# Kernel optimization log

Hardware: AMD Instinct MI355X
Metric: run time of the kernel (lower is better)

The kernel has to match this reference:

```python
import jax, jax.numpy as jnp
import numpy as np

B, N, C, H, PD, CLN = 8, 1024, 512, 8, 256, 64
HD = C // H
HID = 4 * C
LN_EPS = 1e-5
ATT_EPS = 1e-6


def layernorm(x, g, b):
    mu = x.mean(-1, keepdims=True)
    var = ((x - mu) ** 2).mean(-1, keepdims=True)
    return (x - mu) * jax.lax.rsqrt(var + LN_EPS) * g + b


def setup_inputs() -> dict:
    key = jax.random.key(0)
    ks = jax.random.split(key, 16)
    p = lambda k, shp, s=0.02: (jax.random.normal(k, shp, dtype=jnp.float32) * s)
    return {
        "x_token": jax.random.normal(ks[0], (B, N, C), dtype=jnp.float32),
        "x_path": jax.random.normal(ks[1], (B, N, PD), dtype=jnp.float32),
        "wq": p(ks[2], (C, C)),
        "wk": p(ks[3], (C, C)),
        "wv": p(ks[4], (C, C)),
        "w_proj": p(ks[5], (C, C)),
        "b_proj": jnp.zeros((C,), jnp.float32),
        "g1": jnp.ones((C,), jnp.float32),
        "b1": jnp.zeros((C,), jnp.float32),
        "g2": jnp.ones((C,), jnp.float32),
        "b2": jnp.zeros((C,), jnp.float32),
        "w1": p(ks[6], (HID, C)),
        "bb1": jnp.zeros((HID,), jnp.float32),
        "w2": p(ks[7], (C, HID)),
        "bb2": jnp.zeros((C,), jnp.float32),
        "idx_cluster": jax.random.randint(ks[8], (B, N), 0, CLN, dtype=jnp.int64 if jax.config.jax_enable_x64 else jnp.int32),
        "cluster_num": CLN,
    }


def reference(x_token, x_path, wq, wk, wv, w_proj, b_proj, g1, b1, g2, b2,
              w1, bb1, w2, bb2, idx_cluster, cluster_num):
    Bn, Nn, Cn = x_token.shape
    scale = (Cn // H) ** -0.5

    # norm1 + attention
    t = layernorm(x_token, g1, b1)
    q = (t @ wq.T).reshape(Bn, Nn, H, HD).transpose(0, 2, 1, 3)  # bhnd
    k = (t @ wk.T).reshape(Bn, Nn, H, HD).transpose(0, 2, 1, 3)
    v = (t @ wv.T).reshape(Bn, Nn, H, HD).transpose(0, 2, 1, 3)

    # scatter-to-(B,cluster,N,C) then sum over clusters == same-cluster mask on QK^T
    scores = jnp.einsum("bhid,bhjd->bhij", q, k) * scale  # (B,H,N,N)
    same = (idx_cluster[:, None, :, None] == idx_cluster[:, None, None, :])  # (B,1,N,N)
    scores = jnp.where(same, scores, jnp.float32(-1e9))

    # custom eps-stabilized exp-softmax (as in the torch code, no max-subtraction)
    e = jnp.exp(scores.astype(jnp.float32))
    attn = (e + ATT_EPS / Nn) / (e.sum(-1, keepdims=True) + ATT_EPS)

    out = jnp.einsum("bhij,bhjd->bhid", attn, v)
    out = out.transpose(0, 2, 1, 3).reshape(Bn, Nn, Cn)
    out = out @ w_proj.T + b_proj

    x = x_token + out  # drop_path is identity in eval

    # MLP block
    h = layernorm(x, g2, b2)
    m = jax.nn.gelu(h @ w1.T + bb1, approximate=False) @ w2.T + bb2
    return x + m
```

## Files before the change

### kernel.cpp

```cpp
#include <hip/hip_runtime.h>

typedef unsigned short u16;
typedef __attribute__((ext_vector_type(4))) float f32x4;
typedef __attribute__((ext_vector_type(8))) short s16x8;
typedef __attribute__((ext_vector_type(4))) unsigned short u16x4;
typedef __attribute__((ext_vector_type(8))) unsigned short u16x8;

__device__ __forceinline__ u16 f2bf(float f) {
    unsigned int u = __builtin_bit_cast(unsigned int, f);
    u += 0x7fffu + ((u >> 16) & 1u);
    return (u16)(u >> 16);
}
__device__ __forceinline__ float bf2f(u16 h) {
    unsigned int u = ((unsigned int)h) << 16;
    return __builtin_bit_cast(float, u);
}
__device__ __forceinline__ void gload16(const u16* g, u16* l) {
    __builtin_amdgcn_global_load_lds(
        (const __attribute__((address_space(1))) void*)g,
        (__attribute__((address_space(3))) void*)l, 16, 0, 0);
}

__global__ __launch_bounds__(256) void cvt_all(const float* __restrict__ wq,
                                               const float* __restrict__ wk,
                                               const float* __restrict__ wv,
                                               const float* __restrict__ wp,
                                               const float* __restrict__ w1,
                                               const float* __restrict__ w2,
                                               u16* __restrict__ dqkv,
                                               u16* __restrict__ dp,
                                               u16* __restrict__ dw1,
                                               u16* __restrict__ dw2,
                                               float* __restrict__ vsum) {
    int b = blockIdx.x;
    if (b >= 3072) {
        float4 z = {0.f, 0.f, 0.f, 0.f};
        ((float4*)vsum)[(b - 3072) * 256 + threadIdx.x] = z;
        return;
    }
    const float* src; u16* dst; int off;
    if      (b < 256)  { src = wq; dst = dqkv;          off = b; }
    else if (b < 512)  { src = wk; dst = dqkv + 262144; off = b - 256; }
    else if (b < 768)  { src = wv; dst = dqkv + 524288; off = b - 512; }
    else if (b < 1024) { src = wp; dst = dp;            off = b - 768; }
    else if (b < 2048) { src = w1; dst = dw1;           off = b - 1024; }
    else               { src = w2; dst = dw2;           off = b - 2048; }
    int i = off * 256 + threadIdx.x;
    float4 v = ((const float4*)src)[i];
    u16x4 o;
    o.x = f2bf(v.x); o.y = f2bf(v.y); o.z = f2bf(v.z); o.w = f2bf(v.w);
    ((u16x4*)dst)[i] = o;
}

template <bool IN_BF16>
__global__ __launch_bounds__(128) void ln_kernel(const void* __restrict__ inp,
                                                 const float* __restrict__ g,
                                                 const float* __restrict__ bta,
                                                 u16* __restrict__ out) {
    int row = blockIdx.x;
    int t = threadIdx.x;
    float4 v;
    if (IN_BF16) {
        u16x4 hv = ((const u16x4*)inp)[row * 128 + t];
        v.x = bf2f(hv.x); v.y = bf2f(hv.y); v.z = bf2f(hv.z); v.w = bf2f(hv.w);
    } else {
        v = ((const float4*)inp)[row * 128 + t];
    }
    float s  = v.x + v.y + v.z + v.w;
    float s2 = v.x * v.x + v.y * v.y + v.z * v.z + v.w * v.w;
#pragma unroll
    for (int m = 1; m < 64; m <<= 1) { s += __shfl_xor(s, m); s2 += __shfl_xor(s2, m); }
    __shared__ float sh[4];
    if ((t & 63) == 0) { sh[(t >> 6) * 2] = s; sh[(t >> 6) * 2 + 1] = s2; }
    __syncthreads();
    s = sh[0] + sh[2]; s2 = sh[1] + sh[3];
    float mu  = s * (1.0f / 512.0f);
    float var = s2 * (1.0f / 512.0f) - mu * mu;
    float rstd = rsqrtf(var + 1e-5f);
    float4 gv = ((const float4*)g)[t];
    float4 bv = ((const float4*)bta)[t];
    u16x4 o;
    o.x = f2bf((v.x - mu) * rstd * gv.x + bv.x);
    o.y = f2bf((v.y - mu) * rstd * gv.y + bv.y);
    o.z = f2bf((v.z - mu) * rstd * gv.z + bv.z);
    o.w = f2bf((v.w - mu) * rstd * gv.w + bv.w);
    ((u16x4*)(out + (size_t)row * 512))[t] = o;
}

__global__ __launch_bounds__(1024) void cluster_sort(const int* __restrict__ idx,
                                                     int* __restrict__ perm,
                                                     int* __restrict__ cstart,
                                                     int* __restrict__ ccnt) {
    const int b = blockIdx.x, t = threadIdx.x;
    const int w = t >> 6, lane = t & 63;
    __shared__ int whist[16][64];
    __shared__ int cnt[64];
    __shared__ int off[64];
    ((int*)whist)[t] = 0;
    __syncthreads();
    const int myc = idx[b * 1024 + t];
    atomicAdd(&whist[w][myc], 1);
    int rank_w = 0;
    for (int c = 0; c < 64; ++c) {
        unsigned long long m = __ballot(myc == c);
        if (myc == c) rank_w = __popcll(m & ((1ull << lane) - 1ull));
    }
    __syncthreads();
    if (t < 64) {
        int s = 0;
        for (int ww = 0; ww < 16; ++ww) s += whist[ww][t];
        cnt[t] = s;
        ccnt[b * 64 + t] = s;
    }
    __syncthreads();
    if (t == 0) {
        int s = 0;
        for (int c = 0; c < 64; ++c) { off[c] = s; s += cnt[c]; }
    }
    __syncthreads();
    int cross = 0;
    for (int ww = 0; ww < w; ++ww) cross += whist[ww][myc];
    perm[b * 1024 + off[myc] + cross + rank_w] = t;
    if (t < 64) cstart[b * 64 + t] = off[t];
}

__global__ __launch_bounds__(64) void cattn_kernel(const u16* __restrict__ qkv,
                                                   const int* __restrict__ perm,
                                                   const int* __restrict__ cstart,
                                                   const int* __restrict__ ccnt,
                                                   const float* __restrict__ vsum,
                                                   u16* __restrict__ O) {
    const int bid = blockIdx.x;
    const int h = bid & 7, c = (bid >> 3) & 63, b = bid >> 9;
    const int m = ccnt[b * 64 + c];
    if (m == 0) return;
    const int start = b * 1024 + cstart[b * 64 + c];
    const int lane = threadIdx.x;
    const int fr = lane & 15, fkb = lane >> 4;
    __shared__ __align__(16) u16 Qs[16 * 72];
    __shared__ __align__(16) u16 Ks[32 * 72];
    __shared__ __align__(16) u16 Vt[64 * 36];
    __shared__ __align__(16) u16 Pl[16 * 40];

    const u16* qkv_b = qkv + (size_t)b * 1024 * 1536;
    const float epsN = 1e-6f / 1024.0f;

    for (int q0 = 0; q0 < m; q0 += 16) {
        __syncthreads();
        {
            int row = lane >> 3, seg = lane & 7;
#pragma unroll
            for (int p = 0; p < 2; ++p) {
                int r = row + p * 8;
                int gr = perm[start + min(q0 + r, m - 1)];
                *(int4*)(&Qs[r * 72 + seg * 8]) =
                    *(const int4*)(qkv_b + (size_t)gr * 1536 + h * 64 + seg * 8);
            }
        }
        __syncthreads();
        const s16x8 qf0 = *(const s16x8*)(&Qs[fr * 72 + fkb * 8]);
        const s16x8 qf1 = *(const s16x8*)(&Qs[fr * 72 + 32 + fkb * 8]);

        f32x4 oacc[4] = {};
        float rs[4] = {0.f, 0.f, 0.f, 0.f};

        for (int k0 = 0; k0 < m; k0 += 32) {
            __syncthreads();
            {
                int row = lane >> 3, seg = lane & 7;
#pragma unroll
                for (int p = 0; p < 4; ++p) {
                    int r = row + p * 8;
                    int gr = perm[start + min(k0 + r, m - 1)];
                    const u16* src = qkv_b + (size_t)gr * 1536 + h * 64 + seg * 8;
                    *(int4*)(&Ks[r * 72 + seg * 8]) = *(const int4*)(src + 512);
                    u16x8 vv = *(const u16x8*)(src + 1024);
#pragma unroll
                    for (int i = 0; i < 8; ++i) Vt[(seg * 8 + i) * 36 + r] = vv[i];
                }
            }
            __syncthreads();
#pragma unroll
            for (int ct = 0; ct < 2; ++ct) {
                f32x4 sacc = {};
                s16x8 kf0 = *(const s16x8*)(&Ks[(ct * 16 + fr) * 72 + fkb * 8]);
                s16x8 kf1 = *(const s16x8*)(&Ks[(ct * 16 + fr) * 72 + 32 + fkb * 8]);
                sacc = __builtin_amdgcn_mfma_f32_16x16x32_bf16(qf0, kf0, sacc, 0, 0, 0);
                sacc = __builtin_amdgcn_mfma_f32_16x16x32_bf16(qf1, kf1, sacc, 0, 0, 0);
                bool valid = (k0 + ct * 16 + fr) < m;
#pragma unroll
                for (int r = 0; r < 4; ++r) {
                    float e = valid ? __expf(sacc[r] * 0.125f) : 0.0f;
                    rs[r] += e;
                    Pl[(fkb * 4 + r) * 40 + ct * 16 + fr] = f2bf(e);
                }
            }
            __syncthreads();
            s16x8 pf = *(const s16x8*)(&Pl[fr * 40 + fkb * 8]);
#pragma unroll
            for (int dt = 0; dt < 4; ++dt) {
                s16x8 vf = *(const s16x8*)(&Vt[(dt * 16 + fr) * 36 + fkb * 8]);
                oacc[dt] = __builtin_amdgcn_mfma_f32_16x16x32_bf16(pf, vf, oacc[dt], 0, 0, 0);
            }
        }
#pragma unroll
        for (int r = 0; r < 4; ++r)
#pragma unroll
            for (int mm = 1; mm < 16; mm <<= 1) rs[r] += __shfl_xor(rs[r], mm);

#pragma unroll
        for (int r = 0; r < 4; ++r) {
            int ql = q0 + fkb * 4 + r;
            if (ql < m) {
                int orow = perm[start + ql];
#pragma unroll
                for (int dt = 0; dt < 4; ++dt) {
                    int dcol = dt * 16 + fr;
                    float vs = vsum[(b * 8 + h) * 64 + dcol];
                    float val = (oacc[dt][r] + epsN * vs) / (rs[r] + 1e-6f);
                    O[((size_t)(b * 1024 + orow)) * 512 + h * 64 + dcol] = f2bf(val);
                }
            }
        }
    }
}

template <int BM, int BN, bool OUT_BF16, bool BIAS, int RESID, bool GELU, bool VSUM>
__global__ __launch_bounds__(256) void gemm_sb(const u16* __restrict__ A,
                                               const u16* __restrict__ W,
                                               const float* __restrict__ bias,
                                               const void* __restrict__ resid,
                                               void* __restrict__ outp,
                                               float* __restrict__ vsum,
                                               int M, int N, int K) {
    constexpr int MI = BM / 32;
    constexpr int NI = BN / 32;
    __shared__ __align__(16) u16 As[BM * 64];
    __shared__ __align__(16) u16 Bs[BN * 64];
    const int bm = blockIdx.x, bn = blockIdx.y;
    const int t = threadIdx.x;
    const int lane = t & 63, w = t >> 6;
    const int wm = w >> 1, wn = w & 1;
    const int fr = lane & 15, fkb = lane >> 4;
    const int l8 = lane >> 3;
    const int c8s = (((lane & 7) ^ (l8 & 7)) * 8);
    f32x4 acc[MI][NI] = {};
    const u16* Ab = A + (size_t)bm * BM * K;
    const u16* Wb = W + (size_t)bn * BN * K;

    for (int k0 = 0; k0 < K; k0 += 64) {
        __syncthreads();
#pragma unroll
        for (int j = 0; j < MI; ++j) {
            int r = (w * MI + j) * 8 + l8;
            gload16(Ab + (size_t)r * K + k0 + c8s, &As[(w * MI + j) * 512]);
        }
#pragma unroll
        for (int j = 0; j < NI; ++j) {
            int r = (w * NI + j) * 8 + l8;
            gload16(Wb + (size_t)r * K + k0 + c8s, &Bs[(w * NI + j) * 512]);
        }
        __syncthreads();
#pragma unroll
        for (int kk = 0; kk < 64; kk += 32) {
            const int co = (((kk >> 3) + fkb) ^ (fr & 7)) << 3;
            s16x8 af[MI], bfv[NI];
#pragma unroll
            for (int mi = 0; mi < MI; ++mi)
                af[mi] = *(const s16x8*)(&As[(wm * (BM / 2) + mi * 16 + fr) * 64 + co]);
#pragma unroll
            for (int ni = 0; ni < NI; ++ni)
                bfv[ni] = *(const s16x8*)(&Bs[(wn * (BN / 2) + ni * 16 + fr) * 64 + co]);
#pragma unroll
            for (int mi = 0; mi < MI; ++mi)
#pragma unroll
                for (int ni = 0; ni < NI; ++ni)
                    acc[mi][ni] = __builtin_amdgcn_mfma_f32_16x16x32_bf16(
                        af[mi], bfv[ni], acc[mi][ni], 0, 0, 0);
        }
    }

    const int rg = (lane >> 4) * 4;
#pragma unroll
    for (int mi = 0; mi < MI; ++mi) {
#pragma unroll
        for (int ni = 0; ni < NI; ++ni) {
            int gcol = bn * BN + wn * (BN / 2) + ni * 16 + fr;
            float bv = BIAS ? bias[gcol] : 0.0f;
#pragma unroll
            for (int r = 0; r < 4; ++r) {
                int grow = bm * BM + wm * (BM / 2) + mi * 16 + rg + r;
                float v = acc[mi][ni][r] + bv;
                if (GELU) v = 0.5f * v * (1.0f + erff(v * 0.70710678118f));
                if (RESID == 1) v += ((const float*)resid)[(size_t)grow * N + gcol];
                if (RESID == 2) v += bf2f(((const u16*)resid)[(size_t)grow * N + gcol]);
                if (OUT_BF16)
                    ((u16*)outp)[(size_t)grow * N + gcol] = f2bf(v);
                else
                    ((float*)outp)[(size_t)grow * N + gcol] = v;
            }
        }
    }

    if (VSUM && bn * BN >= 1024) {
        const int vb = (bm * BM) >> 10;
#pragma unroll
        for (int ni = 0; ni < NI; ++ni) {
            float p = 0.0f;
#pragma unroll
            for (int mi = 0; mi < MI; ++mi)
#pragma unroll
                for (int r = 0; r < 4; ++r) p += acc[mi][ni][r];
            p += __shfl_xor(p, 16);
            p += __shfl_xor(p, 32);
            if (lane < 16) {
                int gcol = bn * BN + wn * (BN / 2) + ni * 16 + lane;
                atomicAdd(&vsum[vb * 512 + gcol - 1024], p);
            }
        }
    }
}

extern "C" void kernel_launch(void* const* d_in, const int* in_sizes, int n_in,
                              void* d_out, int out_size, void* d_ws, size_t ws_size,
                              hipStream_t stream) {
    const float* x_token = (const float*)d_in[0];
    const float* wq     = (const float*)d_in[2];
    const float* wk     = (const float*)d_in[3];
    const float* wv     = (const float*)d_in[4];
    const float* w_proj = (const float*)d_in[5];
    const float* b_proj = (const float*)d_in[6];
    const float* g1     = (const float*)d_in[7];
    const float* b1     = (const float*)d_in[8];
    const float* g2     = (const float*)d_in[9];
    const float* b2     = (const float*)d_in[10];
    const float* w1     = (const float*)d_in[11];
    const float* bb1    = (const float*)d_in[12];
    const float* w2     = (const float*)d_in[13];
    const float* bb2    = (const float*)d_in[14];
    const int*   idx    = (const int*)d_in[15];
    float* out_f = (float*)d_out;

    char* ws = (char*)d_ws;
    u16*   t_buf = (u16*)(ws);
    u16*   qkv   = (u16*)(ws + 8388608);
    u16*   Obuf  = (u16*)(ws + 8388608 + 25165824);
    u16*   m1    = qkv;
    u16*   x_bf  = (u16*)(ws + 41943040);
    u16*   h_buf = t_buf;
    char*  wsw   = ws + 58720256;
    u16*   wqkv  = (u16*)(wsw);
    u16*   wprjb = (u16*)(wsw + 1572864);
    u16*   w1b   = (u16*)(wsw + 2097152);
    u16*   w2b   = (u16*)(wsw + 4194304);
    float* vsum  = (float*)(wsw + 6291456);
    int*   perm   = (int*)(ws + 41943040);
    int*   cstart = (int*)(ws + 41943040 + 32768);
    int*   ccnt   = (int*)(ws + 41943040 + 34816);
    (void)ws_size; (void)in_sizes; (void)n_in; (void)out_size;

    cvt_all<<<3076, 256, 0, stream>>>(wq, wk, wv, w_proj, w1, w2,
                                      wqkv, wprjb, w1b, w2b, vsum);
    cluster_sort<<<8, 1024, 0, stream>>>(idx, perm, cstart, ccnt);

    ln_kernel<false><<<8192, 128, 0, stream>>>(x_token, g1, b1, t_buf);
    gemm_sb<64, 128, true, false, 0, false, true><<<dim3(128, 12), 256, 0, stream>>>(
        t_buf, wqkv, nullptr, nullptr, qkv, vsum, 8192, 1536, 512);
    cattn_kernel<<<4096, 64, 0, stream>>>(qkv, perm, cstart, ccnt, vsum, Obuf);
    gemm_sb<64, 64, true, true, 1, false, false><<<dim3(128, 8), 256, 0, stream>>>(
        Obuf, wprjb, b_proj, x_token, x_bf, nullptr, 8192, 512, 512);
    ln_kernel<true><<<8192, 128, 0, stream>>>(x_bf, g2, b2, h_buf);
    gemm_sb<64, 128, true, true, 0, true, false><<<dim3(128, 16), 256, 0, stream>>>(
        h_buf, w1b, bb1, nullptr, m1, nullptr, 8192, 2048, 512);
    gemm_sb<64, 64, false, true, 2, false, false><<<dim3(128, 8), 256, 0, stream>>>(
        m1, w2b, bb2, x_bf, out_f, nullptr, 8192, 512, 2048);
}
```

Before: 132.8 us.

## Fuse LN1 into conversion kernel, load Q directly, retile proj GEMM

Folds the first layernorm into the weight-conversion launch as extra blocks, two rows per block. These blocks also emit a bf16 copy of x_token, so the projection GEMM reads a bf16 residual and uses 32-row tiles over twice as many blocks. The attention kernel loads Q fragments straight from global memory into registers, dropping the Q shared-memory stage and two barriers per query tile. This saves a launch and some memory traffic, at the cost of rounding the first residual to bf16, which adds precision error.

```diff
diff --git a/kernel.cpp b/kernel.cpp
--- a/kernel.cpp
+++ b/kernel.cpp
@@ -31,8 +31,45 @@
                                                u16* __restrict__ dp,
                                                u16* __restrict__ dw1,
                                                u16* __restrict__ dw2,
-                                               float* __restrict__ vsum) {
+                                               float* __restrict__ vsum,
+                                               const float* __restrict__ x_token,
+                                               const float* __restrict__ g1,
+                                               const float* __restrict__ b1,
+                                               u16* __restrict__ t_out,
+                                               u16* __restrict__ xtok_bf) {
+    __shared__ float sh[4][2];
     int b = blockIdx.x;
+    if (b >= 3076) {
+        int tid = threadIdx.x;
+        int row = (b - 3076) * 2 + (tid >> 7);
+        int t = tid & 127;
+        float4 v = ((const float4*)(x_token + (size_t)row * 512))[t];
+        float s  = v.x + v.y + v.z + v.w;
+        float s2 = v.x * v.x + v.y * v.y + v.z * v.z + v.w * v.w;
+#pragma unroll
+        for (int m = 1; m < 64; m <<= 1) { s += __shfl_xor(s, m); s2 += __shfl_xor(s2, m); }
+        int w = tid >> 6;
+        if ((tid & 63) == 0) { sh[w][0] = s; sh[w][1] = s2; }
+        __syncthreads();
+        int base = (tid >> 7) * 2;
+        s = sh[base][0] + sh[base + 1][0];
+        s2 = sh[base][1] + sh[base + 1][1];
+        float mu  = s * (1.0f / 512.0f);
+        float var = s2 * (1.0f / 512.0f) - mu * mu;
+        float rstd = rsqrtf(var + 1e-5f);
+        float4 gv = ((const float4*)g1)[t];
+        float4 bv = ((const float4*)b1)[t];
+        u16x4 o;
+        o.x = f2bf((v.x - mu) * rstd * gv.x + bv.x);
+        o.y = f2bf((v.y - mu) * rstd * gv.y + bv.y);
+        o.z = f2bf((v.z - mu) * rstd * gv.z + bv.z);
+        o.w = f2bf((v.w - mu) * rstd * gv.w + bv.w);
+        ((u16x4*)(t_out + (size_t)row * 512))[t] = o;
+        u16x4 xo;
+        xo.x = f2bf(v.x); xo.y = f2bf(v.y); xo.z = f2bf(v.z); xo.w = f2bf(v.w);
+        ((u16x4*)(xtok_bf + (size_t)row * 512))[t] = xo;
+        return;
+    }
     if (b >= 3072) {
         float4 z = {0.f, 0.f, 0.f, 0.f};
         ((float4*)vsum)[(b - 3072) * 256 + threadIdx.x] = z;
@@ -52,20 +89,15 @@
     ((u16x4*)dst)[i] = o;
 }
 
-template <bool IN_BF16>
-__global__ __launch_bounds__(128) void ln_kernel(const void* __restrict__ inp,
+__global__ __launch_bounds__(128) void ln_kernel(const u16* __restrict__ inp,
                                                  const float* __restrict__ g,
                                                  const float* __restrict__ bta,
                                                  u16* __restrict__ out) {
     int row = blockIdx.x;
     int t = threadIdx.x;
+    u16x4 hv = ((const u16x4*)inp)[row * 128 + t];
     float4 v;
-    if (IN_BF16) {
-        u16x4 hv = ((const u16x4*)inp)[row * 128 + t];
-        v.x = bf2f(hv.x); v.y = bf2f(hv.y); v.z = bf2f(hv.z); v.w = bf2f(hv.w);
-    } else {
-        v = ((const float4*)inp)[row * 128 + t];
-    }
+    v.x = bf2f(hv.x); v.y = bf2f(hv.y); v.z = bf2f(hv.z); v.w = bf2f(hv.w);
     float s  = v.x + v.y + v.z + v.w;
     float s2 = v.x * v.x + v.y * v.y + v.z * v.z + v.w * v.w;
 #pragma unroll
@@ -137,7 +169,6 @@
     const int start = b * 1024 + cstart[b * 64 + c];
     const int lane = threadIdx.x;
     const int fr = lane & 15, fkb = lane >> 4;
-    __shared__ __align__(16) u16 Qs[16 * 72];
     __shared__ __align__(16) u16 Ks[32 * 72];
     __shared__ __align__(16) u16 Vt[64 * 36];
     __shared__ __align__(16) u16 Pl[16 * 40];
@@ -146,20 +177,12 @@
     const float epsN = 1e-6f / 1024.0f;
 
     for (int q0 = 0; q0 < m; q0 += 16) {
-        __syncthreads();
         {
-            int row = lane >> 3, seg = lane & 7;
-#pragma unroll
-            for (int p = 0; p < 2; ++p) {
-                int r = row + p * 8;
-                int gr = perm[start + min(q0 + r, m - 1)];
-                *(int4*)(&Qs[r * 72 + seg * 8]) =
-                    *(const int4*)(qkv_b + (size_t)gr * 1536 + h * 64 + seg * 8);
-            }
-        }
-        __syncthreads();
-        const s16x8 qf0 = *(const s16x8*)(&Qs[fr * 72 + fkb * 8]);
-        const s16x8 qf1 = *(const s16x8*)(&Qs[fr * 72 + 32 + fkb * 8]);
+        }
+        const int qgr = perm[start + min(q0 + fr, m - 1)];
+        const u16* qp = qkv_b + (size_t)qgr * 1536 + h * 64 + fkb * 8;
+        const s16x8 qf0 = *(const s16x8*)qp;
+        const s16x8 qf1 = *(const s16x8*)(qp + 32);
 
         f32x4 oacc[4] = {};
         float rs[4] = {0.f, 0.f, 0.f, 0.f};
@@ -342,34 +365,35 @@
     float* out_f = (float*)d_out;
 
     char* ws = (char*)d_ws;
-    u16*   t_buf = (u16*)(ws);
-    u16*   qkv   = (u16*)(ws + 8388608);
-    u16*   Obuf  = (u16*)(ws + 8388608 + 25165824);
-    u16*   m1    = qkv;
-    u16*   x_bf  = (u16*)(ws + 41943040);
-    u16*   h_buf = t_buf;
-    char*  wsw   = ws + 58720256;
-    u16*   wqkv  = (u16*)(wsw);
-    u16*   wprjb = (u16*)(wsw + 1572864);
-    u16*   w1b   = (u16*)(wsw + 2097152);
-    u16*   w2b   = (u16*)(wsw + 4194304);
-    float* vsum  = (float*)(wsw + 6291456);
+    u16*   t_buf   = (u16*)(ws);
+    u16*   qkv     = (u16*)(ws + 8388608);
+    u16*   Obuf    = (u16*)(ws + 8388608 + 25165824);
+    u16*   m1      = qkv;
+    u16*   x_bf    = (u16*)(ws + 41943040);
+    u16*   xtok_bf = (u16*)(ws + 50331648);
+    u16*   h_buf   = t_buf;
+    char*  wsw     = ws + 58720256;
+    u16*   wqkv    = (u16*)(wsw);
+    u16*   wprjb   = (u16*)(wsw + 1572864);
+    u16*   w1b     = (u16*)(wsw + 2097152);
+    u16*   w2b     = (u16*)(wsw + 4194304);
+    float* vsum    = (float*)(wsw + 6291456);
     int*   perm   = (int*)(ws + 41943040);
     int*   cstart = (int*)(ws + 41943040 + 32768);
     int*   ccnt   = (int*)(ws + 41943040 + 34816);
     (void)ws_size; (void)in_sizes; (void)n_in; (void)out_size;
 
-    cvt_all<<<3076, 256, 0, stream>>>(wq, wk, wv, w_proj, w1, w2,
-                                      wqkv, wprjb, w1b, w2b, vsum);
+    cvt_all<<<7172, 256, 0, stream>>>(wq, wk, wv, w_proj, w1, w2,
+                                      wqkv, wprjb, w1b, w2b, vsum,
+                                      x_token, g1, b1, t_buf, xtok_bf);
     cluster_sort<<<8, 1024, 0, stream>>>(idx, perm, cstart, ccnt);
 
-    ln_kernel<false><<<8192, 128, 0, stream>>>(x_token, g1, b1, t_buf);
     gemm_sb<64, 128, true, false, 0, false, true><<<dim3(128, 12), 256, 0, stream>>>(
         t_buf, wqkv, nullptr, nullptr, qkv, vsum, 8192, 1536, 512);
     cattn_kernel<<<4096, 64, 0, stream>>>(qkv, perm, cstart, ccnt, vsum, Obuf);
-    gemm_sb<64, 64, true, true, 1, false, false><<<dim3(128, 8), 256, 0, stream>>>(
-        Obuf, wprjb, b_proj, x_token, x_bf, nullptr, 8192, 512, 512);
-    ln_kernel<true><<<8192, 128, 0, stream>>>(x_bf, g2, b2, h_buf);
+    gemm_sb<32, 64, true, true, 2, false, false><<<dim3(256, 8), 256, 0, stream>>>(
+        Obuf, wprjb, b_proj, xtok_bf, x_bf, nullptr, 8192, 512, 512);
+    ln_kernel<<<8192, 128, 0, stream>>>(x_bf, g2, b2, h_buf);
     gemm_sb<64, 128, true, true, 0, true, false><<<dim3(128, 16), 256, 0, stream>>>(
         h_buf, w1b, bb1, nullptr, m1, nullptr, 8192, 2048, 512);
     gemm_sb<64, 64, false, true, 2, false, false><<<dim3(128, 8), 256, 0, stream>>>(
```

New measurement: 137.8 us. 3.8% more time.
